# Optimization experiments

Measured on AMD Instinct MI355X. Metric: run time of the kernel, lower is better.

Reference implementation:

```python
import jax, jax.numpy as jnp
import numpy as np

def setup_inputs() -> dict:
    key = jax.random.key(0)
    k1, k2, k3, k4, k5 = jax.random.split(key, 5)
    H = 1024
    B, T = 32, 1024
    hidden = jax.random.normal(k1, (1, B, H), dtype=jnp.float32)
    encoder_outputs = jax.random.normal(k2, (B, T, H), dtype=jnp.float32)
    # nn.Linear(2H, H): weight [H, 2H], bias [H]
    bound = 1.0 / np.sqrt(2 * H)
    W = jax.random.uniform(k3, (H, 2 * H), minval=-bound, maxval=bound, dtype=jnp.float32)
    b = jax.random.uniform(k4, (H,), minval=-bound, maxval=bound, dtype=jnp.float32)
    v = jax.random.uniform(k5, (H,), dtype=jnp.float32)  # torch.rand
    return {"hidden": hidden, "encoder_outputs": encoder_outputs, "W": W, "b": b, "v": v}

def reference(hidden, encoder_outputs, W, b, v):
    B = hidden.shape[1]
    H = hidden.shape[2]
    h = jnp.transpose(hidden, (1, 0, 2)).reshape(B, -1)  # [B, H]
    # Split Linear(2H->H): cat([h_rep, enc]) @ W.T == h @ Wh.T + enc @ We.T
    Wh, We = W[:, :H], W[:, H:]
    # [B,1,H] + [B,T,H] -> [B,T,H]
    pre = jnp.tanh((h @ Wh.T + b)[:, None, :] + jnp.einsum('bth,gh->btg', encoder_outputs, We))
    energies = jnp.einsum('bth,h->bt', pre, v)  # [B, T]
    return jax.nn.softmax(energies, axis=1)[:, None, :]  # [B, 1, T]
```

## Files before the change

### kernel.cpp

```cpp
#include <hip/hip_runtime.h>
#include <hip/hip_fp16.h>

typedef _Float16 half8   __attribute__((ext_vector_type(8)));
typedef _Float16 half4_t __attribute__((ext_vector_type(4)));
typedef float    f32x4   __attribute__((ext_vector_type(4)));

#define HDIM  1024
#define BATCH 32
#define TLEN  1024
#define M_TOT (BATCH * TLEN)

#define BM 128
#define BN 128
#define LDA 40

__global__ void prep_k(const float* __restrict__ W, const float* __restrict__ hidden,
                       const float* __restrict__ bias, _Float16* __restrict__ We16,
                       float* __restrict__ q, float* __restrict__ energ) {
    const int bid = blockIdx.x;
    const int t = threadIdx.x;
    if (bid < 1024) {
        int idx = bid * 256 + t;
        int g  = idx >> 8;
        int k4 = idx & 255;
        float4 f = *reinterpret_cast<const float4*>(W + (size_t)g * 2048 + 1024 + k4 * 4);
        half4_t h;
        h[0] = (_Float16)f.x; h[1] = (_Float16)f.y; h[2] = (_Float16)f.z; h[3] = (_Float16)f.w;
        *reinterpret_cast<half4_t*>(We16 + (size_t)idx * 4) = h;
    } else if (bid < 2048) {
        int g = bid - 1024;
        int wave = t >> 6, lane = t & 63;
        float acc[BATCH];
#pragma unroll
        for (int b = 0; b < BATCH; b++) acc[b] = 0.f;
        const float* wr = W + (size_t)g * 2048;
        for (int h = t; h < HDIM; h += 256) {
            float w = wr[h];
#pragma unroll
            for (int b = 0; b < BATCH; b++) acc[b] = fmaf(w, hidden[b * HDIM + h], acc[b]);
        }
        __shared__ float sm[4 * BATCH];
#pragma unroll
        for (int b = 0; b < BATCH; b++) {
            float s = acc[b];
#pragma unroll
            for (int off = 32; off >= 1; off >>= 1) s += __shfl_xor(s, off);
            if (lane == 0) sm[wave * BATCH + b] = s;
        }
        __syncthreads();
        if (t < BATCH) {
            float s = sm[t] + sm[BATCH + t] + sm[2 * BATCH + t] + sm[3 * BATCH + t];
            q[t * HDIM + g] = s + bias[g];
        }
    } else {
        energ[(bid - 2048) * 256 + t] = 0.f;
    }
}

__global__ void enc_convert_k(const float* __restrict__ enc, _Float16* __restrict__ enc16) {
    size_t i = ((size_t)blockIdx.x * blockDim.x + threadIdx.x) * 8;
    float4 f0 = *reinterpret_cast<const float4*>(enc + i);
    float4 f1 = *reinterpret_cast<const float4*>(enc + i + 4);
    half8 h;
    h[0] = (_Float16)f0.x; h[1] = (_Float16)f0.y; h[2] = (_Float16)f0.z; h[3] = (_Float16)f0.w;
    h[4] = (_Float16)f1.x; h[5] = (_Float16)f1.y; h[6] = (_Float16)f1.z; h[7] = (_Float16)f1.w;
    *reinterpret_cast<half8*>(enc16 + i) = h;
}

__device__ __forceinline__ void async16(const void* g, void* l) {
    __builtin_amdgcn_global_load_lds(
        (const __attribute__((address_space(1))) void*)g,
        (__attribute__((address_space(3))) void*)l, 16, 0, 0);
}

#define NIT 8

__global__ __launch_bounds__(512, 2)
void attn_gemm8_k(const _Float16* __restrict__ enc16,
                  const _Float16* __restrict__ We16,
                  const float* __restrict__ q, const float* __restrict__ v,
                  float* __restrict__ energies) {
    __shared__ _Float16 lds[65536];

    const int tid  = threadIdx.x;
    const int id   = blockIdx.x;
    const int xcd  = id & 7;
    const int w    = id >> 3;
    const int m0   = (xcd * 16 + (w >> 2)) * 256;
    const int n0   = (w & 3) * 256;

    const int wave = tid >> 6;
    const int lane = tid & 63;
    const int quad = lane >> 4;
    const int l16  = lane & 15;
    const int wm   = wave >> 2;
    const int wn   = wave & 3;
    const int hb   = wn >> 1;

    const int rA = tid >> 3;
    const int sc = ((tid & 7) ^ (rA & 7)) * 8;
    const _Float16* gA = enc16 + (size_t)(m0 + rA) * HDIM + sc;
    const _Float16* gB = We16  + (size_t)(n0 + rA) * HDIM + sc;

    const int cs0 = (quad ^ (l16 & 7)) * 8;
    const int cs1 = ((4 + quad) ^ (l16 & 7)) * 8;
    const int arow = wm * 8192 + l16 * 64;
    const int brow = 16384 + hb * 8192 + ((wn & 1) * 64 + l16) * 64;

    f32x4 acc[8][4];
#pragma unroll
    for (int i = 0; i < 8; i++)
#pragma unroll
        for (int j = 0; j < 4; j++) acc[i][j] = {0.f, 0.f, 0.f, 0.f};

    half8 aLo[4][2], aHi[4][2], bLo[2][2], bHi[2][2];

#define STAGE_A(buf, ha, kt) do { \
    _Float16* d_ = &lds[(buf)*32768 + (ha)*8192 + tid*8]; \
    const _Float16* s_ = gA + (size_t)(ha)*131072 + (kt)*64; \
    async16(s_, d_); async16(s_ + 65536, d_ + 4096); } while(0)

#define STAGE_B(buf, hbt, kt) do { \
    _Float16* d_ = &lds[(buf)*32768 + 16384 + (hbt)*8192 + tid*8]; \
    const _Float16* s_ = gB + (size_t)(hbt)*131072 + (kt)*64; \
    async16(s_, d_); async16(s_ + 65536, d_ + 4096); } while(0)

#define RD_ALO(bb) { _Pragma("unroll") for (int mi_ = 0; mi_ < 4; mi_++) { \
    aLo[mi_][0] = *reinterpret_cast<const half8*>(&lds[(bb)+arow+mi_*1024+cs0]); \
    aLo[mi_][1] = *reinterpret_cast<const half8*>(&lds[(bb)+arow+mi_*1024+cs1]); } }
#define RD_AHI(bb) { _Pragma("unroll") for (int mi_ = 0; mi_ < 4; mi_++) { \
    aHi[mi_][0] = *reinterpret_cast<const half8*>(&lds[(bb)+arow+(mi_+4)*1024+cs0]); \
    aHi[mi_][1] = *reinterpret_cast<const half8*>(&lds[(bb)+arow+(mi_+4)*1024+cs1]); } }
#define RD_BLO(bb) { _Pragma("unroll") for (int ni_ = 0; ni_ < 2; ni_++) { \
    bLo[ni_][0] = *reinterpret_cast<const half8*>(&lds[(bb)+brow+ni_*1024+cs0]); \
    bLo[ni_][1] = *reinterpret_cast<const half8*>(&lds[(bb)+brow+ni_*1024+cs1]); } }
#define RD_BHI(bb) { _Pragma("unroll") for (int ni_ = 0; ni_ < 2; ni_++) { \
    bHi[ni_][0] = *reinterpret_cast<const half8*>(&lds[(bb)+brow+(ni_+2)*1024+cs0]); \
    bHi[ni_][1] = *reinterpret_cast<const half8*>(&lds[(bb)+brow+(ni_+2)*1024+cs1]); } }

#define MFMA16(AF, BF, MO, NO) { _Pragma("unroll") for (int ks_ = 0; ks_ < 2; ks_++) \
    _Pragma("unroll") for (int mi_ = 0; mi_ < 4; mi_++) \
    _Pragma("unroll") for (int ni_ = 0; ni_ < 2; ni_++) \
      acc[mi_+MO][ni_+NO] = __builtin_amdgcn_mfma_f32_16x16x32_f16( \
          AF[mi_][ks_], BF[ni_][ks_], acc[mi_+MO][ni_+NO], 0, 0, 0); }

#define BAR1 { __builtin_amdgcn_s_barrier(); \
    asm volatile("s_waitcnt lgkmcnt(0)" ::: "memory"); \
    __builtin_amdgcn_sched_barrier(0); \
    __builtin_amdgcn_s_setprio(1); }
#define BAR2 { __builtin_amdgcn_s_setprio(0); \
    __builtin_amdgcn_s_barrier(); \
    __builtin_amdgcn_sched_barrier(0); }
#define BAR2V(n) { __builtin_amdgcn_s_setprio(0); \
    asm volatile("s_waitcnt vmcnt(" #n ")" ::: "memory"); \
    __builtin_amdgcn_s_barrier(); \
    __builtin_amdgcn_sched_barrier(0); }

    STAGE_A(0, 0, 0); STAGE_A(0, 1, 0); STAGE_B(0, 0, 0); STAGE_B(0, 1, 0);
    STAGE_B(1, 0, 1); STAGE_B(1, 1, 1);
    asm volatile("s_waitcnt vmcnt(4)" ::: "memory");
    __builtin_amdgcn_s_barrier();
    __builtin_amdgcn_sched_barrier(0);

    for (int i = 0; i < NIT; i++) {
        const int kt1 = 2 * i + 1, kt2 = 2 * i + 2, kt3 = 2 * i + 3;
        const bool more = (i < NIT - 1);
        RD_ALO(0); RD_BLO(0);            STAGE_A(1, 0, kt1);
        BAR1; MFMA16(aLo, bLo, 0, 0); BAR2;
        RD_BHI(0);                       STAGE_A(1, 1, kt1);
        BAR1; MFMA16(aLo, bHi, 0, 2); BAR2;
        RD_AHI(0);                       if (more) STAGE_B(0, 0, kt2);
        BAR1; MFMA16(aHi, bHi, 4, 2); BAR2;
                                         if (more) STAGE_B(0, 1, kt2);
        BAR1; MFMA16(aHi, bLo, 4, 0);
        if (more) { BAR2V(4); } else { BAR2V(0); }
        RD_ALO(32768); RD_BLO(32768);    if (more) STAGE_A(0, 0, kt2);
        BAR1; MFMA16(aLo, bLo, 0, 0); BAR2;
        RD_BHI(32768);                   if (more) STAGE_A(0, 1, kt2);
        BAR1; MFMA16(aLo, bHi, 0, 2); BAR2;
        RD_AHI(32768);                   if (more) STAGE_B(1, 0, kt3);
        BAR1; MFMA16(aHi, bHi, 4, 2); BAR2;
                                         if (more) STAGE_B(1, 1, kt3);
        BAR1; MFMA16(aHi, bLo, 4, 0);
        if (more) { BAR2V(4); } else { BAR2; }
    }

    const int bidx = m0 >> 10;
    const int gb = n0 + wn * 64;
    float qv[4], vv[4];
#pragma unroll
    for (int ni = 0; ni < 4; ni++) {
        int g = gb + ni * 16 + l16;
        qv[ni] = q[bidx * HDIM + g];
        vv[ni] = v[g];
    }
#pragma unroll
    for (int mi = 0; mi < 8; mi++) {
#pragma unroll
        for (int r = 0; r < 4; r++) {
            int row = m0 + wm * 128 + mi * 16 + quad * 4 + r;
            float s = 0.f;
#pragma unroll
            for (int ni = 0; ni < 4; ni++) {
                float pre = acc[mi][ni][r] + qv[ni];
                float e = __expf(2.f * pre);
                float th = 1.f - 2.f / (e + 1.f);
                s = fmaf(th, vv[ni], s);
            }
            s += __shfl_xor(s, 1);
            s += __shfl_xor(s, 2);
            s += __shfl_xor(s, 4);
            s += __shfl_xor(s, 8);
            if (l16 == 0) atomicAdd(&energies[row], s);
        }
    }
#undef STAGE_A
#undef STAGE_B
#undef RD_ALO
#undef RD_AHI
#undef RD_BLO
#undef RD_BHI
#undef MFMA16
#undef BAR1
#undef BAR2
#undef BAR2V
}

__global__ __launch_bounds__(256, 2)
void attn_gemm_k(const float* __restrict__ enc, const _Float16* __restrict__ We16,
                 const float* __restrict__ q, const float* __restrict__ v,
                 float* __restrict__ energies) {
    __shared__ _Float16 As[BM * LDA];
    __shared__ _Float16 Bs[BN * LDA];

    const int tid  = threadIdx.x;
    const int m0   = blockIdx.x * BM;
    const int n0   = blockIdx.y * BN;
    const int wave = tid >> 6;
    const int lane = tid & 63;
    const int quad = lane >> 4;
    const int l16  = lane & 15;
    const int wm   = (wave & 1) * 64;
    const int wn   = (wave >> 1) * 64;

    const int srow = tid >> 1;
    const int scol = (tid & 1) * 16;

    f32x4 acc[4][4];
#pragma unroll
    for (int i = 0; i < 4; i++)
#pragma unroll
        for (int j = 0; j < 4; j++) acc[i][j] = {0.f, 0.f, 0.f, 0.f};

    const float*    ag = enc  + (size_t)(m0 + srow) * HDIM + scol;
    const _Float16* bg = We16 + (size_t)(n0 + srow) * HDIM + scol;
    _Float16* aw = &As[srow * LDA + scol];
    _Float16* bw = &Bs[srow * LDA + scol];

    for (int k0 = 0; k0 < HDIM; k0 += 32) {
        float4 a0 = *reinterpret_cast<const float4*>(ag + k0 + 0);
        float4 a1 = *reinterpret_cast<const float4*>(ag + k0 + 4);
        float4 a2 = *reinterpret_cast<const float4*>(ag + k0 + 8);
        float4 a3 = *reinterpret_cast<const float4*>(ag + k0 + 12);
        float4 b0 = *reinterpret_cast<const float4*>(bg + k0);
        float4 b1 = *reinterpret_cast<const float4*>(bg + k0 + 8);

        __syncthreads();

        half8 ha0, ha1;
        ha0[0] = (_Float16)a0.x; ha0[1] = (_Float16)a0.y; ha0[2] = (_Float16)a0.z; ha0[3] = (_Float16)a0.w;
        ha0[4] = (_Float16)a1.x; ha0[5] = (_Float16)a1.y; ha0[6] = (_Float16)a1.z; ha0[7] = (_Float16)a1.w;
        ha1[0] = (_Float16)a2.x; ha1[1] = (_Float16)a2.y; ha1[2] = (_Float16)a2.z; ha1[3] = (_Float16)a2.w;
        ha1[4] = (_Float16)a3.x; ha1[5] = (_Float16)a3.y; ha1[6] = (_Float16)a3.z; ha1[7] = (_Float16)a3.w;
        *reinterpret_cast<half8*>(aw)     = ha0;
        *reinterpret_cast<half8*>(aw + 8) = ha1;
        *reinterpret_cast<float4*>(bw)     = b0;
        *reinterpret_cast<float4*>(bw + 8) = b1;

        __syncthreads();

        half8 af[4], bf[4];
#pragma unroll
        for (int i = 0; i < 4; i++) {
            af[i] = *reinterpret_cast<const half8*>(&As[(wm + i * 16 + l16) * LDA + quad * 8]);
            bf[i] = *reinterpret_cast<const half8*>(&Bs[(wn + i * 16 + l16) * LDA + quad * 8]);
        }
#pragma unroll
        for (int mi = 0; mi < 4; mi++)
#pragma unroll
            for (int ni = 0; ni < 4; ni++)
                acc[mi][ni] = __builtin_amdgcn_mfma_f32_16x16x32_f16(af[mi], bf[ni], acc[mi][ni], 0, 0, 0);
    }

    const int bidx = m0 >> 10;
    float qv[4], vv[4];
#pragma unroll
    for (int ni = 0; ni < 4; ni++) {
        int g = n0 + wn + ni * 16 + l16;
        qv[ni] = q[bidx * HDIM + g];
        vv[ni] = v[g];
    }
#pragma unroll
    for (int mi = 0; mi < 4; mi++) {
#pragma unroll
        for (int r = 0; r < 4; r++) {
            int row = wm + mi * 16 + quad * 4 + r;
            float s = 0.f;
#pragma unroll
            for (int ni = 0; ni < 4; ni++) {
                float pre = acc[mi][ni][r] + qv[ni];
                float e = __expf(2.f * pre);
                float th = 1.f - 2.f / (e + 1.f);
                s = fmaf(th, vv[ni], s);
            }
            s += __shfl_xor(s, 1);
            s += __shfl_xor(s, 2);
            s += __shfl_xor(s, 4);
            s += __shfl_xor(s, 8);
            if (l16 == 0) atomicAdd(&energies[m0 + row], s);
        }
    }
}

__global__ void softmax_k(const float* __restrict__ energies, float* __restrict__ out) {
    int b = blockIdx.x;
    int t = threadIdx.x;
    int wave = t >> 6, lane = t & 63;
    __shared__ float smax[4], ssum[4];
    float e[4];
#pragma unroll
    for (int i = 0; i < 4; i++) e[i] = energies[b * TLEN + t + i * 256];
    float m = fmaxf(fmaxf(e[0], e[1]), fmaxf(e[2], e[3]));
#pragma unroll
    for (int off = 32; off >= 1; off >>= 1) m = fmaxf(m, __shfl_xor(m, off));
    if (lane == 0) smax[wave] = m;
    __syncthreads();
    float M = fmaxf(fmaxf(smax[0], smax[1]), fmaxf(smax[2], smax[3]));
    float x[4]; float s = 0.f;
#pragma unroll
    for (int i = 0; i < 4; i++) { x[i] = __expf(e[i] - M); s += x[i]; }
#pragma unroll
    for (int off = 32; off >= 1; off >>= 1) s += __shfl_xor(s, off);
    if (lane == 0) ssum[wave] = s;
    __syncthreads();
    float S = ssum[0] + ssum[1] + ssum[2] + ssum[3];
    float inv = 1.f / S;
#pragma unroll
    for (int i = 0; i < 4; i++) out[b * TLEN + t + i * 256] = x[i] * inv;
}

extern "C" void kernel_launch(void* const* d_in, const int* in_sizes, int n_in,
                              void* d_out, int out_size, void* d_ws, size_t ws_size,
                              hipStream_t stream) {
    const float* hidden = (const float*)d_in[0];
    const float* enc    = (const float*)d_in[1];
    const float* W      = (const float*)d_in[2];
    const float* bias   = (const float*)d_in[3];
    const float* v      = (const float*)d_in[4];
    float* out = (float*)d_out;

    char* ws = (char*)d_ws;
    float*    q     = (float*)ws;
    float*    energ = (float*)(ws + 131072);
    _Float16* We16  = (_Float16*)(ws + 262144);
    _Float16* enc16 = (_Float16*)(ws + 262144 + 2097152);
    const size_t need_fast = 262144 + 2097152 + (size_t)M_TOT * HDIM * 2;

    prep_k<<<dim3(2176), 256, 0, stream>>>(W, hidden, bias, We16, q, energ);
    if (ws_size >= need_fast) {
        enc_convert_k<<<dim3((size_t)M_TOT * HDIM / 8 / 256), 256, 0, stream>>>(enc, enc16);
        attn_gemm8_k<<<dim3(512), 512, 0, stream>>>(enc16, We16, q, v, energ);
    } else {
        attn_gemm_k<<<dim3(256, 8), 256, 0, stream>>>(enc, We16, q, v, energ);
    }
    softmax_k<<<dim3(BATCH), 256, 0, stream>>>(energ, out);
}
```

Before: 306.0 us.

## Fuse enc conversion into prep kernel, replace atomics with partial-sum buffer, retune GEMM pipeline

Merges the fp32-to-fp16 conversion of encoder outputs into the prep kernel, which removes one launch and the energies zeroing pass. The GEMM now writes per-column-block partial energies into a [M,16] buffer instead of doing atomicAdd, and the softmax sums those 16 partials. The GEMM main loop's staging order is reworked: A is double-buffered by halves, fragment registers are reduced to a single aF/bF set, and an lgkmcnt wait is added. The launch-bounds minimum of 2 blocks per CU is dropped. The cost is a larger workspace and more softmax reads.

```diff
diff --git a/kernel.cpp b/kernel.cpp
--- a/kernel.cpp
+++ b/kernel.cpp
@@ -15,8 +15,9 @@
 #define LDA 40
 
 __global__ void prep_k(const float* __restrict__ W, const float* __restrict__ hidden,
-                       const float* __restrict__ bias, _Float16* __restrict__ We16,
-                       float* __restrict__ q, float* __restrict__ energ) {
+                       const float* __restrict__ bias, const float* __restrict__ enc,
+                       _Float16* __restrict__ We16, float* __restrict__ q,
+                       _Float16* __restrict__ enc16) {
     const int bid = blockIdx.x;
     const int t = threadIdx.x;
     if (bid < 1024) {
@@ -53,18 +54,14 @@
             q[t * HDIM + g] = s + bias[g];
         }
     } else {
-        energ[(bid - 2048) * 256 + t] = 0.f;
-    }
-}
-
-__global__ void enc_convert_k(const float* __restrict__ enc, _Float16* __restrict__ enc16) {
-    size_t i = ((size_t)blockIdx.x * blockDim.x + threadIdx.x) * 8;
-    float4 f0 = *reinterpret_cast<const float4*>(enc + i);
-    float4 f1 = *reinterpret_cast<const float4*>(enc + i + 4);
-    half8 h;
-    h[0] = (_Float16)f0.x; h[1] = (_Float16)f0.y; h[2] = (_Float16)f0.z; h[3] = (_Float16)f0.w;
-    h[4] = (_Float16)f1.x; h[5] = (_Float16)f1.y; h[6] = (_Float16)f1.z; h[7] = (_Float16)f1.w;
-    *reinterpret_cast<half8*>(enc16 + i) = h;
+        size_t i = ((size_t)(bid - 2048) * 256 + t) * 8;
+        float4 f0 = *reinterpret_cast<const float4*>(enc + i);
+        float4 f1 = *reinterpret_cast<const float4*>(enc + i + 4);
+        half8 h;
+        h[0] = (_Float16)f0.x; h[1] = (_Float16)f0.y; h[2] = (_Float16)f0.z; h[3] = (_Float16)f0.w;
+        h[4] = (_Float16)f1.x; h[5] = (_Float16)f1.y; h[6] = (_Float16)f1.z; h[7] = (_Float16)f1.w;
+        *reinterpret_cast<half8*>(enc16 + i) = h;
+    }
 }
 
 __device__ __forceinline__ void async16(const void* g, void* l) {
@@ -75,11 +72,11 @@
 
 #define NIT 8
 
-__global__ __launch_bounds__(512, 2)
+__global__ __launch_bounds__(512)
 void attn_gemm8_k(const _Float16* __restrict__ enc16,
                   const _Float16* __restrict__ We16,
                   const float* __restrict__ q, const float* __restrict__ v,
-                  float* __restrict__ energies) {
+                  float* __restrict__ energ) {
     __shared__ _Float16 lds[65536];
 
     const int tid  = threadIdx.x;
@@ -87,7 +84,8 @@
     const int xcd  = id & 7;
     const int w    = id >> 3;
     const int m0   = (xcd * 16 + (w >> 2)) * 256;
-    const int n0   = (w & 3) * 256;
+    const int nblk = w & 3;
+    const int n0   = nblk * 256;
 
     const int wave = tid >> 6;
     const int lane = tid & 63;
@@ -113,77 +111,84 @@
 #pragma unroll
         for (int j = 0; j < 4; j++) acc[i][j] = {0.f, 0.f, 0.f, 0.f};
 
-    half8 aLo[4][2], aHi[4][2], bLo[2][2], bHi[2][2];
-
-#define STAGE_A(buf, ha, kt) do { \
+    half8 aF[4][2], bF[2][2];
+
+#define STAGE_AH(buf, ha, kt) { \
     _Float16* d_ = &lds[(buf)*32768 + (ha)*8192 + tid*8]; \
     const _Float16* s_ = gA + (size_t)(ha)*131072 + (kt)*64; \
-    async16(s_, d_); async16(s_ + 65536, d_ + 4096); } while(0)
-
-#define STAGE_B(buf, hbt, kt) do { \
-    _Float16* d_ = &lds[(buf)*32768 + 16384 + (hbt)*8192 + tid*8]; \
-    const _Float16* s_ = gB + (size_t)(hbt)*131072 + (kt)*64; \
-    async16(s_, d_); async16(s_ + 65536, d_ + 4096); } while(0)
-
-#define RD_ALO(bb) { _Pragma("unroll") for (int mi_ = 0; mi_ < 4; mi_++) { \
-    aLo[mi_][0] = *reinterpret_cast<const half8*>(&lds[(bb)+arow+mi_*1024+cs0]); \
-    aLo[mi_][1] = *reinterpret_cast<const half8*>(&lds[(bb)+arow+mi_*1024+cs1]); } }
-#define RD_AHI(bb) { _Pragma("unroll") for (int mi_ = 0; mi_ < 4; mi_++) { \
-    aHi[mi_][0] = *reinterpret_cast<const half8*>(&lds[(bb)+arow+(mi_+4)*1024+cs0]); \
-    aHi[mi_][1] = *reinterpret_cast<const half8*>(&lds[(bb)+arow+(mi_+4)*1024+cs1]); } }
-#define RD_BLO(bb) { _Pragma("unroll") for (int ni_ = 0; ni_ < 2; ni_++) { \
-    bLo[ni_][0] = *reinterpret_cast<const half8*>(&lds[(bb)+brow+ni_*1024+cs0]); \
-    bLo[ni_][1] = *reinterpret_cast<const half8*>(&lds[(bb)+brow+ni_*1024+cs1]); } }
-#define RD_BHI(bb) { _Pragma("unroll") for (int ni_ = 0; ni_ < 2; ni_++) { \
-    bHi[ni_][0] = *reinterpret_cast<const half8*>(&lds[(bb)+brow+(ni_+2)*1024+cs0]); \
-    bHi[ni_][1] = *reinterpret_cast<const half8*>(&lds[(bb)+brow+(ni_+2)*1024+cs1]); } }
-
-#define MFMA16(AF, BF, MO, NO) { _Pragma("unroll") for (int ks_ = 0; ks_ < 2; ks_++) \
+    async16(s_, d_); async16(s_ + 65536, d_ + 4096); }
+
+#define STAGE_BH(buf, hh, kt) { \
+    _Float16* d_ = &lds[(buf)*32768 + 16384 + (hh)*8192 + tid*8]; \
+    const _Float16* s_ = gB + (size_t)(hh)*131072 + (kt)*64; \
+    async16(s_, d_); async16(s_ + 65536, d_ + 4096); }
+
+#define RD_A(bb, HO) { _Pragma("unroll") for (int mi_ = 0; mi_ < 4; mi_++) { \
+    aF[mi_][0] = *reinterpret_cast<const half8*>(&lds[(bb)+arow+(mi_+HO)*1024+cs0]); \
+    aF[mi_][1] = *reinterpret_cast<const half8*>(&lds[(bb)+arow+(mi_+HO)*1024+cs1]); } }
+
+#define RD_B(bb, HO) { _Pragma("unroll") for (int ni_ = 0; ni_ < 2; ni_++) { \
+    bF[ni_][0] = *reinterpret_cast<const half8*>(&lds[(bb)+brow+(ni_+HO)*1024+cs0]); \
+    bF[ni_][1] = *reinterpret_cast<const half8*>(&lds[(bb)+brow+(ni_+HO)*1024+cs1]); } }
+
+#define MFMA16(MO, NO) { _Pragma("unroll") for (int ks_ = 0; ks_ < 2; ks_++) \
     _Pragma("unroll") for (int mi_ = 0; mi_ < 4; mi_++) \
     _Pragma("unroll") for (int ni_ = 0; ni_ < 2; ni_++) \
       acc[mi_+MO][ni_+NO] = __builtin_amdgcn_mfma_f32_16x16x32_f16( \
-          AF[mi_][ks_], BF[ni_][ks_], acc[mi_+MO][ni_+NO], 0, 0, 0); }
-
-#define BAR1 { __builtin_amdgcn_s_barrier(); \
+          aF[mi_][ks_], bF[ni_][ks_], acc[mi_+MO][ni_+NO], 0, 0, 0); }
+
+#define PH_MID { __builtin_amdgcn_s_barrier(); \
     asm volatile("s_waitcnt lgkmcnt(0)" ::: "memory"); \
     __builtin_amdgcn_sched_barrier(0); \
     __builtin_amdgcn_s_setprio(1); }
-#define BAR2 { __builtin_amdgcn_s_setprio(0); \
+#define PH_END { __builtin_amdgcn_s_setprio(0); \
     __builtin_amdgcn_s_barrier(); \
     __builtin_amdgcn_sched_barrier(0); }
-#define BAR2V(n) { __builtin_amdgcn_s_setprio(0); \
-    asm volatile("s_waitcnt vmcnt(" #n ")" ::: "memory"); \
-    __builtin_amdgcn_s_barrier(); \
-    __builtin_amdgcn_sched_barrier(0); }
-
-    STAGE_A(0, 0, 0); STAGE_A(0, 1, 0); STAGE_B(0, 0, 0); STAGE_B(0, 1, 0);
-    STAGE_B(1, 0, 1); STAGE_B(1, 1, 1);
+
+    STAGE_AH(0, 0, 0); STAGE_AH(0, 1, 0); STAGE_BH(0, 0, 0); STAGE_BH(0, 1, 0);
+    STAGE_AH(1, 0, 1); STAGE_AH(1, 1, 1);
     asm volatile("s_waitcnt vmcnt(4)" ::: "memory");
     __builtin_amdgcn_s_barrier();
     __builtin_amdgcn_sched_barrier(0);
 
     for (int i = 0; i < NIT; i++) {
-        const int kt1 = 2 * i + 1, kt2 = 2 * i + 2, kt3 = 2 * i + 3;
         const bool more = (i < NIT - 1);
-        RD_ALO(0); RD_BLO(0);            STAGE_A(1, 0, kt1);
-        BAR1; MFMA16(aLo, bLo, 0, 0); BAR2;
-        RD_BHI(0);                       STAGE_A(1, 1, kt1);
-        BAR1; MFMA16(aLo, bHi, 0, 2); BAR2;
-        RD_AHI(0);                       if (more) STAGE_B(0, 0, kt2);
-        BAR1; MFMA16(aHi, bHi, 4, 2); BAR2;
-                                         if (more) STAGE_B(0, 1, kt2);
-        BAR1; MFMA16(aHi, bLo, 4, 0);
-        if (more) { BAR2V(4); } else { BAR2V(0); }
-        RD_ALO(32768); RD_BLO(32768);    if (more) STAGE_A(0, 0, kt2);
-        BAR1; MFMA16(aLo, bLo, 0, 0); BAR2;
-        RD_BHI(32768);                   if (more) STAGE_A(0, 1, kt2);
-        BAR1; MFMA16(aLo, bHi, 0, 2); BAR2;
-        RD_AHI(32768);                   if (more) STAGE_B(1, 0, kt3);
-        BAR1; MFMA16(aHi, bHi, 4, 2); BAR2;
-                                         if (more) STAGE_B(1, 1, kt3);
-        BAR1; MFMA16(aHi, bLo, 4, 0);
-        if (more) { BAR2V(4); } else { BAR2; }
-    }
+        const int t1 = 2 * i + 1, t2 = 2 * i + 2, t3 = 2 * i + 3;
+        RD_A(0, 0); RD_B(0, 0);  STAGE_BH(1, 0, t1);
+        asm volatile("s_waitcnt lgkmcnt(8)" ::: "memory");
+        PH_MID; MFMA16(0, 0); PH_END;
+        RD_B(0, 2);              STAGE_BH(1, 1, t1);
+        PH_MID; MFMA16(0, 2); PH_END;
+        RD_A(0, 4);
+        PH_MID; MFMA16(4, 2); PH_END;
+        RD_B(0, 0);              if (more) { STAGE_AH(0, 0, t2); STAGE_AH(0, 1, t2); }
+        PH_MID; MFMA16(4, 0);
+        __builtin_amdgcn_s_setprio(0);
+        if (more) { asm volatile("s_waitcnt vmcnt(4)" ::: "memory"); }
+        else      { asm volatile("s_waitcnt vmcnt(0)" ::: "memory"); }
+        __builtin_amdgcn_s_barrier();
+        __builtin_amdgcn_sched_barrier(0);
+        RD_A(32768, 0); RD_B(32768, 0);  if (more) STAGE_BH(0, 0, t2);
+        asm volatile("s_waitcnt lgkmcnt(8)" ::: "memory");
+        PH_MID; MFMA16(0, 0); PH_END;
+        RD_B(32768, 2);                  if (more) STAGE_BH(0, 1, t2);
+        PH_MID; MFMA16(0, 2); PH_END;
+        RD_A(32768, 4);
+        PH_MID; MFMA16(4, 2); PH_END;
+        RD_B(32768, 0);                  if (more) { STAGE_AH(1, 0, t3); STAGE_AH(1, 1, t3); }
+        PH_MID; MFMA16(4, 0);
+        __builtin_amdgcn_s_setprio(0);
+        if (more) { asm volatile("s_waitcnt vmcnt(4)" ::: "memory"); }
+        __builtin_amdgcn_s_barrier();
+        __builtin_amdgcn_sched_barrier(0);
+    }
+#undef STAGE_AH
+#undef STAGE_BH
+#undef RD_A
+#undef RD_B
+#undef MFMA16
+#undef PH_MID
+#undef PH_END
 
     const int bidx = m0 >> 10;
     const int gb = n0 + wn * 64;
@@ -211,25 +216,15 @@
             s += __shfl_xor(s, 2);
             s += __shfl_xor(s, 4);
             s += __shfl_xor(s, 8);
-            if (l16 == 0) atomicAdd(&energies[row], s);
-        }
-    }
-#undef STAGE_A
-#undef STAGE_B
-#undef RD_ALO
-#undef RD_AHI
-#undef RD_BLO
-#undef RD_BHI
-#undef MFMA16
-#undef BAR1
-#undef BAR2
-#undef BAR2V
+            if (l16 == 0) energ[(size_t)row * 16 + nblk * 4 + wn] = s;
+        }
+    }
 }
 
 __global__ __launch_bounds__(256, 2)
 void attn_gemm_k(const float* __restrict__ enc, const _Float16* __restrict__ We16,
                  const float* __restrict__ q, const float* __restrict__ v,
-                 float* __restrict__ energies) {
+                 float* __restrict__ energ) {
     __shared__ _Float16 As[BM * LDA];
     __shared__ _Float16 Bs[BN * LDA];
 
@@ -293,6 +288,7 @@
     }
 
     const int bidx = m0 >> 10;
+    const int half = wn >> 6;
     float qv[4], vv[4];
 #pragma unroll
     for (int ni = 0; ni < 4; ni++) {
@@ -317,19 +313,28 @@
             s += __shfl_xor(s, 2);
             s += __shfl_xor(s, 4);
             s += __shfl_xor(s, 8);
-            if (l16 == 0) atomicAdd(&energies[m0 + row], s);
-        }
-    }
-}
-
-__global__ void softmax_k(const float* __restrict__ energies, float* __restrict__ out) {
+            if (l16 == 0) energ[(size_t)(m0 + row) * 16 + blockIdx.y * 2 + half] = s;
+        }
+    }
+}
+
+__global__ void softmax_k(const float* __restrict__ energ, float* __restrict__ out) {
     int b = blockIdx.x;
     int t = threadIdx.x;
     int wave = t >> 6, lane = t & 63;
     __shared__ float smax[4], ssum[4];
     float e[4];
 #pragma unroll
-    for (int i = 0; i < 4; i++) e[i] = energies[b * TLEN + t + i * 256];
+    for (int i = 0; i < 4; i++) {
+        size_t m = (size_t)b * TLEN + t + i * 256;
+        const float* p = energ + m * 16;
+        f32x4 p0 = *reinterpret_cast<const f32x4*>(p);
+        f32x4 p1 = *reinterpret_cast<const f32x4*>(p + 4);
+        f32x4 p2 = *reinterpret_cast<const f32x4*>(p + 8);
+        f32x4 p3 = *reinterpret_cast<const f32x4*>(p + 12);
+        e[i] = ((p0[0] + p0[1]) + (p0[2] + p0[3])) + ((p1[0] + p1[1]) + (p1[2] + p1[3]))
+             + ((p2[0] + p2[1]) + (p2[2] + p2[3])) + ((p3[0] + p3[1]) + (p3[2] + p3[3]));
+    }
     float m = fmaxf(fmaxf(e[0], e[1]), fmaxf(e[2], e[3]));
 #pragma unroll
     for (int off = 32; off >= 1; off >>= 1) m = fmaxf(m, __shfl_xor(m, off));
@@ -362,15 +367,15 @@
     char* ws = (char*)d_ws;
     float*    q     = (float*)ws;
     float*    energ = (float*)(ws + 131072);
-    _Float16* We16  = (_Float16*)(ws + 262144);
-    _Float16* enc16 = (_Float16*)(ws + 262144 + 2097152);
-    const size_t need_fast = 262144 + 2097152 + (size_t)M_TOT * HDIM * 2;
-
-    prep_k<<<dim3(2176), 256, 0, stream>>>(W, hidden, bias, We16, q, energ);
+    _Float16* We16  = (_Float16*)(ws + 131072 + 2097152);
+    _Float16* enc16 = (_Float16*)(ws + 131072 + 2097152 + 2097152);
+    const size_t need_fast = 131072 + 2097152 + 2097152 + (size_t)M_TOT * HDIM * 2;
+
     if (ws_size >= need_fast) {
-        enc_convert_k<<<dim3((size_t)M_TOT * HDIM / 8 / 256), 256, 0, stream>>>(enc, enc16);
+        prep_k<<<dim3(18432), 256, 0, stream>>>(W, hidden, bias, enc, We16, q, enc16);
         attn_gemm8_k<<<dim3(512), 512, 0, stream>>>(enc16, We16, q, v, energ);
     } else {
+        prep_k<<<dim3(2048), 256, 0, stream>>>(W, hidden, bias, enc, We16, q, enc16);
         attn_gemm_k<<<dim3(256, 8), 256, 0, stream>>>(enc, We16, q, v, energ);
     }
     softmax_k<<<dim3(BATCH), 256, 0, stream>>>(energ, out);
```

Measured after the change: 294.1 us. 3.9% less time.
